# Performance work log

Measured on AMD Instinct MI355X. Metric: run time of the kernel, lower is better.

The kernel has to match this reference:

```python
import jax, jax.numpy as jnp
import numpy as np

D = 1024
EXPAND = 2
DI = EXPAND * D
K = 4           # d_conv
C = 64          # chunk_size
ALPHA = 0.9     # memory decay
B, S = 2, 8192
EPS = 1e-5


def setup_inputs() -> dict:
    key = jax.random.key(0)
    ks = jax.random.split(key, 10)
    s = 0.02
    return {
        "x": jax.random.normal(ks[0], (B, S, D), dtype=jnp.float32),
        "norm_w": jnp.ones((D,), dtype=jnp.float32),
        "w_up": jax.random.normal(ks[1], (D, DI), dtype=jnp.float32) * s,
        "w_gate": jax.random.normal(ks[2], (D, DI), dtype=jnp.float32) * s,
        "w_down": jax.random.normal(ks[3], (DI, D), dtype=jnp.float32) * s,
        "conv_w": jax.random.normal(ks[4], (K, 1, DI), dtype=jnp.float32) * s,  # WIO depthwise
        "conv_b": jnp.zeros((DI,), dtype=jnp.float32),
        "wq": jax.random.normal(ks[5], (D, D), dtype=jnp.float32) * s,
        "wk": jax.random.normal(ks[6], (D, D), dtype=jnp.float32) * s,
        "wv": jax.random.normal(ks[7], (D, D), dtype=jnp.float32) * s,
        "wo": jax.random.normal(ks[8], (D, D), dtype=jnp.float32) * s,
    }


def _rmsnorm(x, w):
    ms = jnp.mean(jnp.square(x.astype(jnp.float32)), axis=-1, keepdims=True)
    return (x * jax.lax.rsqrt(ms + EPS).astype(x.dtype)) * w


def _causal_depthwise_conv(u, conv_w, conv_b):
    # u: [B,S,DI]; depthwise causal conv over S, then SiLU
    y = jax.lax.conv_general_dilated(
        u, conv_w,
        window_strides=(1,), padding=[(K - 1, 0)],
        dimension_numbers=("NWC", "WIO", "NWC"),
        feature_group_count=DI)
    return jax.nn.silu(y + conv_b)


def _hebbian_memory(h, wq, wk, wv, wo):
    # chunked linear-attention style Hebbian memory
    b, s, d = h.shape
    n = s // C
    scale = d ** -0.5
    q = (h @ wq).reshape(b, n, C, d) * scale
    k = (h @ wk).reshape(b, n, C, d)
    v = (h @ wv).reshape(b, n, C, d)
    mask = jnp.tril(jnp.ones((C, C), dtype=h.dtype))  # inclusive causal within chunk

    def step(M, qkv):
        qc, kc, vc = qkv  # [b,C,d]
        inter = jnp.einsum("bcd,bde->bce", qc, M)
        attn = jnp.einsum("bcd,bed->bce", qc, kc) * mask
        intra = jnp.einsum("bce,bed->bcd", attn, vc)
        M_new = ALPHA * M + jnp.einsum("bcd,bce->bde", kc, vc)
        return M_new, inter + intra

    M0 = jnp.zeros((b, d, d), dtype=h.dtype)
    qkv = (jnp.swapaxes(q, 0, 1), jnp.swapaxes(k, 0, 1), jnp.swapaxes(v, 0, 1))
    _, o = jax.lax.scan(step, M0, qkv)        # [n,b,C,d]
    o = jnp.swapaxes(o, 0, 1).reshape(b, s, d)
    return o @ wo


def reference(x, norm_w, w_up, w_gate, w_down, conv_w, conv_b, wq, wk, wv, wo):
    normed = _rmsnorm(x, norm_w)
    val = _causal_depthwise_conv(normed @ w_up, conv_w, conv_b)   # [B,S,DI]
    gate = jax.nn.silu(normed @ w_gate)
    out = (gate * val) @ w_down                                   # [B,S,D]
    out = _hebbian_memory(out, wq, wk, wv, wo)
    return x + out
```

## Files before the change

### kernel.cpp

```cpp
#include <hip/hip_runtime.h>
#include <cstdint>
#include <cstddef>

#define SS 8192
#define DD 1024
#define DI2 2048
#define NR 16384

#define LOG2_09 (-0.152003093445050f)
#define LAMBDA16 0.185302018885184f

typedef __attribute__((ext_vector_type(4))) float f32x4;
typedef __attribute__((ext_vector_type(8))) __bf16 bf16x8;

union U16 { uint4 u; bf16x8 b; };

static __device__ __forceinline__ f32x4 MFMA(uint4 a, uint4 b, f32x4 c) {
  U16 ua, ub; ua.u = a; ub.u = b;
  return __builtin_amdgcn_mfma_f32_16x16x32_bf16(ua.b, ub.b, c, 0, 0, 0);
}

static __device__ __forceinline__ unsigned short f2bf(float f) {
  union { float f; unsigned u; } v; v.f = f;
  return (unsigned short)((v.u + 0x7FFFu + ((v.u >> 16) & 1u)) >> 16);
}
static __device__ __forceinline__ float bf2f(unsigned b) {
  union { unsigned u; float f; } v; v.u = b << 16; return v.f;
}
static __device__ __forceinline__ void unpack8(uint4 u, float* f) {
  f[0] = bf2f(u.x & 0xFFFFu); f[1] = bf2f(u.x >> 16);
  f[2] = bf2f(u.y & 0xFFFFu); f[3] = bf2f(u.y >> 16);
  f[4] = bf2f(u.z & 0xFFFFu); f[5] = bf2f(u.z >> 16);
  f[6] = bf2f(u.w & 0xFFFFu); f[7] = bf2f(u.w >> 16);
}

static __device__ __forceinline__ void glds16(const unsigned short* g, char* l) {
  __builtin_amdgcn_global_load_lds(
      (const __attribute__((address_space(1))) unsigned int*)g,
      (__attribute__((address_space(3))) unsigned int*)l, 16, 0, 0);
}

__global__ __launch_bounds__(256)
void transpose_cast(const float* __restrict__ in, unsigned short* __restrict__ out, int R, int Cc) {
  __shared__ float tile[32][33];
  const int r0 = blockIdx.y * 32, c0 = blockIdx.x * 32;
  const int tx = threadIdx.x, ty = threadIdx.y;
#pragma unroll
  for (int i = 0; i < 4; i++)
    tile[ty + i * 8][tx] = in[(size_t)(r0 + ty + i * 8) * Cc + c0 + tx];
  __syncthreads();
#pragma unroll
  for (int i = 0; i < 4; i++)
    out[(size_t)(c0 + ty + i * 8) * R + r0 + tx] = f2bf(tile[tx][ty + i * 8]);
}

__global__ __launch_bounds__(256)
void rmsnorm_kernel(const float* __restrict__ x, const float* __restrict__ w,
                    unsigned short* __restrict__ out) {
  const int row = blockIdx.x, t = threadIdx.x;
  const float4 v = ((const float4*)(x + (size_t)row * DD))[t];
  float ss = v.x * v.x + v.y * v.y + v.z * v.z + v.w * v.w;
  __shared__ float sred[256];
  sred[t] = ss;
  __syncthreads();
  for (int o = 128; o > 0; o >>= 1) {
    if (t < o) sred[t] += sred[t + o];
    __syncthreads();
  }
  const float rr = rsqrtf(sred[0] * (1.0f / (float)DD) + 1e-5f);
  const float4 wv = ((const float4*)w)[t];
  uint2 pk;
  pk.x = (unsigned)f2bf(v.x * rr * wv.x) | ((unsigned)f2bf(v.y * rr * wv.y) << 16);
  pk.y = (unsigned)f2bf(v.z * rr * wv.z) | ((unsigned)f2bf(v.w * rr * wv.w) << 16);
  *(uint2*)(out + (size_t)row * DD + t * 4) = pk;
}

enum { EP_BF16 = 0, EP_BF16_BOTH = 1, EP_BF16_T = 2, EP_F32_RES = 3, EP_STATE = 4,
       EP_CROSS = 5, EP_SCORE = 6, EP_PV = 7, EP_QKV = 8 };

template <int MODE>
__global__ __launch_bounds__(512, 2)
void gemm256(const unsigned short* __restrict__ A, const unsigned short* __restrict__ Bt,
             unsigned short* __restrict__ Cb, unsigned short* __restrict__ Ct,
             float* __restrict__ Cf, const float* __restrict__ resid,
             int M, int N, int kLen, int lda, int ldb, float scale) {
  __shared__ char sLds[131072];
  const int t = threadIdx.x, lane = t & 63, wid = t >> 6;
  const int wr = wid >> 2, wc = wid & 3;
  const int l15 = lane & 15, lh = lane >> 4;
  const int mblocks = M >> 8;
  int m0, n0;
  if constexpr (MODE == EP_SCORE) {
    const int p = (int)blockIdx.x;
    const int mt = (p >= 6) ? 3 : (p >= 3) ? 2 : (p >= 1) ? 1 : 0;
    const int nt = p - ((mt * (mt + 1)) >> 1);
    m0 = mt << 8; n0 = nt << 8;
  } else if ((mblocks & 7) == 0) {
    const int msl = mblocks >> 3;
    const int xcd = (int)blockIdx.x & 7, loc = (int)blockIdx.x >> 3;
    m0 = (xcd * msl + (loc % msl)) << 8;
    n0 = (loc / msl) << 8;
  } else {
    m0 = ((int)blockIdx.x % mblocks) << 8;
    n0 = ((int)blockIdx.x / mblocks) << 8;
  }
  int zb = 0, zg = 0;
  const unsigned short* Abase = A;
  const unsigned short* Bbase = Bt;
  if constexpr (MODE == EP_STATE || MODE == EP_CROSS || MODE == EP_SCORE || MODE == EP_PV) {
    const int gb = blockIdx.z;
    zb = gb >> 3; zg = gb & 7;
    if constexpr (MODE == EP_STATE) {
      Abase = A + (size_t)zb * DD * SS + (size_t)zg * 1024;
      Bbase = Bt + (size_t)zb * DD * SS + (size_t)zg * 1024;
    } else if constexpr (MODE == EP_CROSS) {
      Abase = A + ((size_t)zb * SS + (size_t)zg * 1024) * (size_t)lda;
      Bbase = Bt + ((size_t)blockIdx.z << 20);
    } else if constexpr (MODE == EP_SCORE) {
      Abase = A + ((size_t)zb * SS + (size_t)zg * 1024) * (size_t)lda;
      Bbase = Bt + ((size_t)zb * SS + (size_t)zg * 1024) * (size_t)ldb;
    } else {
      Abase = A + ((size_t)blockIdx.z << 20);
      Bbase = Bt + (size_t)zb * DD * SS + (size_t)zg * 1024;
    }
  }
  const int srow = wid * 16 + (lane >> 2);
  const int scol = ((lane & 3) << 3) ^ (((srow >> 1) & 3) << 3);
  const unsigned short* pA0 = Abase + (size_t)(m0 + srow) * lda + scol;
  const unsigned short* pA1 = pA0 + (size_t)128 * lda;
  const unsigned short* pB0 = Bbase + (size_t)(n0 + srow) * ldb + scol;
  const unsigned short* pB1 = pB0 + (size_t)128 * ldb;
  const int ldsW = wid * 1024;
  int offA[8], offB[4];
#pragma unroll
  for (int mf = 0; mf < 8; mf++) {
    const int r = wr * 128 + mf * 16 + l15;
    offA[mf] = r * 64 + ((lh * 16) ^ (((r >> 1) & 3) << 4));
  }
#pragma unroll
  for (int nf = 0; nf < 4; nf++) {
    const int r = wc * 64 + nf * 16 + l15;
    offB[nf] = r * 64 + ((lh * 16) ^ (((r >> 1) & 3) << 4));
  }
  int NT = kLen >> 5;
  if constexpr (MODE == EP_PV) NT = ((m0 >> 8) + 1) << 3;
#define BUFA(tt) (sLds + ((tt) & 3) * 32768)
#define BUFB(tt) (sLds + ((tt) & 3) * 32768 + 16384)
#define STAGEA(tt) do { const int _k = (tt) * 32; \
    glds16(pA0 + _k, BUFA(tt) + ldsW); \
    glds16(pA1 + _k, BUFA(tt) + 8192 + ldsW); } while (0)
#define STAGEB(tt) do { const int _k = (tt) * 32; \
    glds16(pB0 + _k, BUFB(tt) + ldsW); \
    glds16(pB1 + _k, BUFB(tt) + 8192 + ldsW); } while (0)
  STAGEA(0); STAGEB(0); STAGEA(1); STAGEB(1); STAGEA(2); STAGEB(2);
  asm volatile("s_waitcnt vmcnt(8)" ::: "memory");
  __builtin_amdgcn_s_barrier();
  f32x4 acc[8][4] = {};
  for (int kt = 0; kt < NT; ++kt) {
    const char* At  = BUFA(kt);
    const char* Bt_ = BUFB(kt);
    uint4 av[8], bv[4];
#pragma unroll
    for (int i = 0; i < 8; i++) av[i] = *(const uint4*)(At + offA[i]);
#pragma unroll
    for (int i = 0; i < 4; i++) bv[i] = *(const uint4*)(Bt_ + offB[i]);
    if (kt + 3 < NT) { STAGEA(kt + 3); STAGEB(kt + 3); }
    __builtin_amdgcn_s_setprio(1);
#pragma unroll
    for (int mf = 0; mf < 8; mf++)
#pragma unroll
      for (int nf = 0; nf < 4; nf++)
        acc[mf][nf] = MFMA(av[mf], bv[nf], acc[mf][nf]);
    __builtin_amdgcn_s_setprio(0);
    if (kt < NT - 3)       { asm volatile("s_waitcnt vmcnt(8)" ::: "memory"); }
    else if (kt == NT - 3) { asm volatile("s_waitcnt vmcnt(4)" ::: "memory"); }
    else if (kt == NT - 2) { asm volatile("s_waitcnt vmcnt(0)" ::: "memory"); }
    __builtin_amdgcn_s_barrier();
  }
#undef STAGEA
#undef STAGEB
#undef BUFA
#undef BUFB
#pragma unroll
  for (int mf = 0; mf < 8; mf++) {
    const int r0 = m0 + wr * 128 + mf * 16 + lh * 4;
#pragma unroll
    for (int nf = 0; nf < 4; nf++) {
      const int c = n0 + wc * 64 + nf * 16 + l15;
      f32x4 v = acc[mf][nf] * scale;
      if constexpr (MODE == EP_F32_RES) {
#pragma unroll
        for (int jj = 0; jj < 4; jj++) {
          const size_t idx = (size_t)(r0 + jj) * N + c;
          Cf[idx] = v[jj] + resid[idx];
        }
      } else if constexpr (MODE == EP_STATE) {
        unsigned short* Tg = Cb + ((size_t)blockIdx.z << 20);
#pragma unroll
        for (int jj = 0; jj < 4; jj++)
          Tg[(size_t)(r0 + jj) * 1024 + c] = f2bf(v[jj]);
      } else if constexpr (MODE == EP_CROSS) {
        const float rs = exp2f((float)(r0 >> 6) * LOG2_09);
#pragma unroll
        for (int jj = 0; jj < 4; jj++) {
          const size_t idx = ((size_t)zb * SS + (size_t)zg * 1024 + r0 + jj) * DD + c;
          Cb[idx] = f2bf(bf2f(Cb[idx]) + v[jj] * rs);
        }
      } else if constexpr (MODE == EP_SCORE) {
        unsigned short* Sg = Cb + ((size_t)blockIdx.z << 20);
        const int qt = r0 >> 6;
        const int tb = c >> 6;
        float w;
        if (tb > qt)       w = 0.0f;
        else if (tb == qt) w = 1.0f;
        else               w = exp2f((float)(qt - 1 - tb) * LOG2_09);
#pragma unroll
        for (int jj = 0; jj < 4; jj++) {
          float val = v[jj] * w;
          if (tb == qt && (c & 63) > ((r0 + jj) & 63)) val = 0.0f;
          Sg[(size_t)(r0 + jj) * 1024 + c] = f2bf(val);
        }
      } else if constexpr (MODE == EP_PV) {
#pragma unroll
        for (int jj = 0; jj < 4; jj++)
          Cb[((size_t)zb * SS + (size_t)zg * 1024 + r0 + jj) * DD + c] = f2bf(v[jj]);
      } else if constexpr (MODE == EP_QKV) {
        unsigned short* qb  = Cb;
        unsigned short* kb  = Ct;
        unsigned short* ktb = (unsigned short*)Cf;
        unsigned short* vtb = (unsigned short*)const_cast<float*>(resid);
        const int sect = c >> 10, cc = c & 1023;
        const int bb = r0 >> 13, s0 = r0 & (SS - 1);
        if (sect == 0) {
#pragma unroll
          for (int jj = 0; jj < 4; jj++)
            qb[(size_t)(r0 + jj) * DD + cc] = f2bf(v[jj] * 0.03125f);
        } else if (sect == 1) {
#pragma unroll
          for (int jj = 0; jj < 4; jj++)
            kb[(size_t)(r0 + jj) * DD + cc] = f2bf(v[jj]);
          const float wt = exp2f((float)(15 - ((s0 >> 6) & 15)) * LOG2_09);
          uint2 pk;
          pk.x = (unsigned)f2bf(v[0] * wt) | ((unsigned)f2bf(v[1] * wt) << 16);
          pk.y = (unsigned)f2bf(v[2] * wt) | ((unsigned)f2bf(v[3] * wt) << 16);
          *(uint2*)(ktb + ((size_t)bb * DD + cc) * SS + s0) = pk;
        } else {
          uint2 pk;
          pk.x = (unsigned)f2bf(v[0]) | ((unsigned)f2bf(v[1]) << 16);
          pk.y = (unsigned)f2bf(v[2]) | ((unsigned)f2bf(v[3]) << 16);
          *(uint2*)(vtb + ((size_t)bb * DD + cc) * SS + s0) = pk;
        }
      } else {
        if constexpr (MODE == EP_BF16 || MODE == EP_BF16_BOTH) {
#pragma unroll
          for (int jj = 0; jj < 4; jj++)
            Cb[(size_t)(r0 + jj) * N + c] = f2bf(v[jj]);
        }
        if constexpr (MODE == EP_BF16_BOTH || MODE == EP_BF16_T) {
          const int bb = r0 >> 13, s0 = r0 & (SS - 1);
          float wt = 1.0f;
          if constexpr (MODE == EP_BF16_BOTH)
            wt = exp2f((float)(15 - ((s0 >> 6) & 15)) * LOG2_09);
          uint2 pk;
          pk.x = (unsigned)f2bf(v[0] * wt) | ((unsigned)f2bf(v[1] * wt) << 16);
          pk.y = (unsigned)f2bf(v[2] * wt) | ((unsigned)f2bf(v[3] * wt) << 16);
          *(uint2*)(Ct + ((size_t)bb * DD + c) * SS + s0) = pk;
        }
      }
    }
  }
}

__global__ __launch_bounds__(256)
void convgate_kernel(const unsigned short* __restrict__ ug, const float* __restrict__ cw,
                     const float* __restrict__ cb, unsigned short* __restrict__ hin) {
  const int r = blockIdx.x;
  const int c0 = threadIdx.x * 8;
  const int s = r & (SS - 1);
  float acc[8];
#pragma unroll
  for (int i = 0; i < 8; i++) acc[i] = cb[c0 + i];
  for (int tap = 0; tap < 4; tap++) {
    const int ds = s - 3 + tap;
    if (ds < 0) continue;
    uint4 uv = *(const uint4*)(ug + (size_t)(r - 3 + tap) * 4096 + c0);
    float u[8]; unpack8(uv, u);
#pragma unroll
    for (int i = 0; i < 8; i++) acc[i] += u[i] * cw[tap * DI2 + c0 + i];
  }
  uint4 gv = *(const uint4*)(ug + (size_t)r * 4096 + DI2 + c0);
  float gt[8]; unpack8(gv, gt);
  unsigned short o16[8];
#pragma unroll
  for (int i = 0; i < 8; i++) {
    const float val = acc[i] / (1.0f + __expf(-acc[i]));
    const float gg  = gt[i] / (1.0f + __expf(-gt[i]));
    o16[i] = f2bf(val * gg);
  }
  uint4 ov;
  ov.x = (unsigned)o16[0] | ((unsigned)o16[1] << 16);
  ov.y = (unsigned)o16[2] | ((unsigned)o16[3] << 16);
  ov.z = (unsigned)o16[4] | ((unsigned)o16[5] << 16);
  ov.w = (unsigned)o16[6] | ((unsigned)o16[7] << 16);
  *(uint4*)(hin + (size_t)r * DI2 + c0) = ov;
}

__global__ __launch_bounds__(256)
void prefix_kernel(unsigned short* __restrict__ Tb) {
  const int tid = blockIdx.x * 256 + threadIdx.x;
  const int b = tid >> 17, i = tid & 131071;
  unsigned short* p = Tb + (((size_t)b * 8) << 20) + (size_t)i * 8;
  float acc[8] = {};
  for (int g = 0; g < 8; g++) {
    unsigned short* pg = p + ((size_t)g << 20);
    uint4 tv = *(uint4*)pg;
    float tf_[8]; unpack8(tv, tf_);
    uint4 ov;
    ov.x = (unsigned)f2bf(acc[0]) | ((unsigned)f2bf(acc[1]) << 16);
    ov.y = (unsigned)f2bf(acc[2]) | ((unsigned)f2bf(acc[3]) << 16);
    ov.z = (unsigned)f2bf(acc[4]) | ((unsigned)f2bf(acc[5]) << 16);
    ov.w = (unsigned)f2bf(acc[6]) | ((unsigned)f2bf(acc[7]) << 16);
    *(uint4*)pg = ov;
#pragma unroll
    for (int e = 0; e < 8; e++) acc[e] = LAMBDA16 * acc[e] + tf_[e];
  }
}

extern "C" void kernel_launch(void* const* d_in, const int* in_sizes, int n_in,
                              void* d_out, int out_size, void* d_ws, size_t ws_size,
                              hipStream_t stream) {
  (void)in_sizes; (void)n_in; (void)out_size;
  const float* x      = (const float*)d_in[0];
  const float* norm_w = (const float*)d_in[1];
  const float* w_up   = (const float*)d_in[2];
  const float* w_gate = (const float*)d_in[3];
  const float* w_down = (const float*)d_in[4];
  const float* conv_w = (const float*)d_in[5];
  const float* conv_b = (const float*)d_in[6];
  const float* wq     = (const float*)d_in[7];
  const float* wk     = (const float*)d_in[8];
  const float* wv     = (const float*)d_in[9];
  const float* wo     = (const float*)d_in[10];
  float* out = (float*)d_out;

  const size_t MB = 1ull << 20;
  if (ws_size < 212 * MB) return;
  char* base = (char*)d_ws;
  unsigned short* ug     = (unsigned short*)(base + 0);
  unsigned short* hbuf   = (unsigned short*)(base + 0);
  unsigned short* Tbuf   = (unsigned short*)(base + 0);
  unsigned short* qbuf   = (unsigned short*)(base + 32 * MB);
  unsigned short* kbuf   = (unsigned short*)(base + 64 * MB);
  unsigned short* ktbuf  = (unsigned short*)(base + 96 * MB);
  unsigned short* sbuf   = (unsigned short*)(base + 96 * MB);
  unsigned short* normed = (unsigned short*)(base + 128 * MB);
  unsigned short* hin    = (unsigned short*)(base + 128 * MB);
  unsigned short* vtbuf  = (unsigned short*)(base + 128 * MB);
  unsigned short* obuf   = (unsigned short*)(base + 160 * MB);
  unsigned short* wugt   = (unsigned short*)(base + 192 * MB);
  unsigned short* wdt    = (unsigned short*)(base + 200 * MB);
  unsigned short* wqkvt  = (unsigned short*)(base + 204 * MB);
  unsigned short* wot    = (unsigned short*)(base + 210 * MB);

  dim3 tb(32, 8);
  transpose_cast<<<dim3(DI2 / 32, DD / 32), tb, 0, stream>>>(w_up,   wugt,                    DD,  DI2);
  transpose_cast<<<dim3(DI2 / 32, DD / 32), tb, 0, stream>>>(w_gate, wugt + (size_t)DI2 * DD, DD,  DI2);
  transpose_cast<<<dim3(DD / 32, DI2 / 32), tb, 0, stream>>>(w_down, wdt, DI2, DD);
  transpose_cast<<<dim3(DD / 32, DD / 32),  tb, 0, stream>>>(wq, wqkvt,                          DD, DD);
  transpose_cast<<<dim3(DD / 32, DD / 32),  tb, 0, stream>>>(wk, wqkvt + (size_t)DD * DD,       DD, DD);
  transpose_cast<<<dim3(DD / 32, DD / 32),  tb, 0, stream>>>(wv, wqkvt + (size_t)2 * DD * DD,   DD, DD);
  transpose_cast<<<dim3(DD / 32, DD / 32),  tb, 0, stream>>>(wo, wot, DD, DD);

  rmsnorm_kernel<<<NR, 256, 0, stream>>>(x, norm_w, normed);

  gemm256<EP_BF16><<<dim3((NR / 256) * (4096 / 256)), 512, 0, stream>>>(
      normed, wugt, ug, nullptr, nullptr, nullptr, NR, 4096, DD, DD, DD, 1.0f);

  convgate_kernel<<<NR, 256, 0, stream>>>(ug, conv_w, conv_b, hin);

  gemm256<EP_BF16><<<dim3((NR / 256) * (DD / 256)), 512, 0, stream>>>(
      hin, wdt, hbuf, nullptr, nullptr, nullptr, NR, DD, DI2, DI2, DI2, 1.0f);

  gemm256<EP_QKV><<<dim3((NR / 256) * (3072 / 256)), 512, 0, stream>>>(
      hbuf, wqkvt, qbuf, kbuf, (float*)ktbuf, (const float*)vtbuf,
      NR, 3072, DD, DD, DD, 1.0f);

  gemm256<EP_STATE><<<dim3(16, 1, 16), 512, 0, stream>>>(
      vtbuf, ktbuf, Tbuf, nullptr, nullptr, nullptr, 1024, 1024, 1024, SS, SS, 1.0f);
  gemm256<EP_SCORE><<<dim3(10, 1, 16), 512, 0, stream>>>(
      qbuf, kbuf, sbuf, nullptr, nullptr, nullptr, 1024, 1024, 1024, DD, DD, 1.0f);
  prefix_kernel<<<1024, 256, 0, stream>>>(Tbuf);
  gemm256<EP_PV><<<dim3(16, 1, 16), 512, 0, stream>>>(
      sbuf, vtbuf, obuf, nullptr, nullptr, nullptr, 1024, 1024, 1024, 1024, SS, 1.0f);
  gemm256<EP_CROSS><<<dim3(16, 1, 16), 512, 0, stream>>>(
      qbuf, Tbuf, obuf, nullptr, nullptr, nullptr, 1024, 1024, 1024, DD, 1024, 1.0f);

  gemm256<EP_F32_RES><<<dim3((NR / 256) * (DD / 256)), 512, 0, stream>>>(
      obuf, wot, nullptr, nullptr, out, x, NR, DD, DD, DD, DD, 1.0f);
}
```

Baseline: 669.1 us.

## Fuse cross-group state GEMM into PV GEMM by concatenating K dimension

The separate EP_CROSS GEMM, which read-modify-wrote the output with a decay-scaled q·T product, is folded into the PV GEMM. The K loop is extended by 32 tiles that stage a pre-decayed q copy and the prefix state instead of scores and V. To make this work, the QKV epilogue now also writes a decay-weighted scaled q (qsbuf). This removes one kernel launch and the bf16 read-modify-write pass over the output, at the cost of an extra q write and some buffer reassignments that reuse workspace regions.

```diff
diff --git a/kernel.cpp b/kernel.cpp
--- a/kernel.cpp
+++ b/kernel.cpp
@@ -76,13 +76,14 @@
 }
 
 enum { EP_BF16 = 0, EP_BF16_BOTH = 1, EP_BF16_T = 2, EP_F32_RES = 3, EP_STATE = 4,
-       EP_CROSS = 5, EP_SCORE = 6, EP_PV = 7, EP_QKV = 8 };
+       EP_SCORE = 6, EP_PVX = 7, EP_QKV = 8 };
 
 template <int MODE>
 __global__ __launch_bounds__(512, 2)
 void gemm256(const unsigned short* __restrict__ A, const unsigned short* __restrict__ Bt,
              unsigned short* __restrict__ Cb, unsigned short* __restrict__ Ct,
              float* __restrict__ Cf, const float* __restrict__ resid,
+             unsigned short* __restrict__ Cx,
              int M, int N, int kLen, int lda, int ldb, float scale) {
   __shared__ char sLds[131072];
   const int t = threadIdx.x, lane = t & 63, wid = t >> 6;
@@ -107,15 +108,12 @@
   int zb = 0, zg = 0;
   const unsigned short* Abase = A;
   const unsigned short* Bbase = Bt;
-  if constexpr (MODE == EP_STATE || MODE == EP_CROSS || MODE == EP_SCORE || MODE == EP_PV) {
+  if constexpr (MODE == EP_STATE || MODE == EP_SCORE || MODE == EP_PVX) {
     const int gb = blockIdx.z;
     zb = gb >> 3; zg = gb & 7;
     if constexpr (MODE == EP_STATE) {
       Abase = A + (size_t)zb * DD * SS + (size_t)zg * 1024;
       Bbase = Bt + (size_t)zb * DD * SS + (size_t)zg * 1024;
-    } else if constexpr (MODE == EP_CROSS) {
-      Abase = A + ((size_t)zb * SS + (size_t)zg * 1024) * (size_t)lda;
-      Bbase = Bt + ((size_t)blockIdx.z << 20);
     } else if constexpr (MODE == EP_SCORE) {
       Abase = A + ((size_t)zb * SS + (size_t)zg * 1024) * (size_t)lda;
       Bbase = Bt + ((size_t)zb * SS + (size_t)zg * 1024) * (size_t)ldb;
@@ -131,6 +129,17 @@
   const unsigned short* pB0 = Bbase + (size_t)(n0 + srow) * ldb + scol;
   const unsigned short* pB1 = pB0 + (size_t)128 * ldb;
   const int ldsW = wid * 1024;
+  int ntV = 0;
+  const unsigned short *pA2 = nullptr, *pA2h = nullptr, *pB2 = nullptr, *pB2h = nullptr;
+  if constexpr (MODE == EP_PVX) {
+    ntV = ((m0 >> 8) + 1) << 3;
+    const unsigned short* qsb = Cx + ((size_t)zb * SS + (size_t)zg * 1024) * DD;
+    pA2  = qsb + (size_t)(m0 + srow) * DD + scol;
+    pA2h = pA2 + (size_t)128 * DD;
+    const unsigned short* mnb = Ct + ((size_t)blockIdx.z << 20);
+    pB2  = mnb + (size_t)(n0 + srow) * 1024 + scol;
+    pB2h = pB2 + (size_t)128 * 1024;
+  }
   int offA[8], offB[4];
 #pragma unroll
   for (int mf = 0; mf < 8; mf++) {
@@ -143,16 +152,28 @@
     offB[nf] = r * 64 + ((lh * 16) ^ (((r >> 1) & 3) << 4));
   }
   int NT = kLen >> 5;
-  if constexpr (MODE == EP_PV) NT = ((m0 >> 8) + 1) << 3;
+  if constexpr (MODE == EP_PVX) NT = ntV + 32;
 #define BUFA(tt) (sLds + ((tt) & 3) * 32768)
 #define BUFB(tt) (sLds + ((tt) & 3) * 32768 + 16384)
-#define STAGEA(tt) do { const int _k = (tt) * 32; \
-    glds16(pA0 + _k, BUFA(tt) + ldsW); \
-    glds16(pA1 + _k, BUFA(tt) + 8192 + ldsW); } while (0)
-#define STAGEB(tt) do { const int _k = (tt) * 32; \
-    glds16(pB0 + _k, BUFB(tt) + ldsW); \
-    glds16(pB1 + _k, BUFB(tt) + 8192 + ldsW); } while (0)
-  STAGEA(0); STAGEB(0); STAGEA(1); STAGEB(1); STAGEA(2); STAGEB(2);
+  auto stage = [&](int tt) {
+    const int _k = tt * 32;
+    const unsigned short* a0 = pA0 + _k;
+    const unsigned short* a1 = pA1 + _k;
+    const unsigned short* b0 = pB0 + _k;
+    const unsigned short* b1 = pB1 + _k;
+    if constexpr (MODE == EP_PVX) {
+      if (tt >= ntV) {
+        const int k2 = (tt - ntV) * 32;
+        a0 = pA2 + k2; a1 = pA2h + k2;
+        b0 = pB2 + k2; b1 = pB2h + k2;
+      }
+    }
+    glds16(a0, BUFA(tt) + ldsW);
+    glds16(a1, BUFA(tt) + 8192 + ldsW);
+    glds16(b0, BUFB(tt) + ldsW);
+    glds16(b1, BUFB(tt) + 8192 + ldsW);
+  };
+  stage(0); stage(1); stage(2);
   asm volatile("s_waitcnt vmcnt(8)" ::: "memory");
   __builtin_amdgcn_s_barrier();
   f32x4 acc[8][4] = {};
@@ -164,7 +185,7 @@
     for (int i = 0; i < 8; i++) av[i] = *(const uint4*)(At + offA[i]);
 #pragma unroll
     for (int i = 0; i < 4; i++) bv[i] = *(const uint4*)(Bt_ + offB[i]);
-    if (kt + 3 < NT) { STAGEA(kt + 3); STAGEB(kt + 3); }
+    if (kt + 3 < NT) stage(kt + 3);
     __builtin_amdgcn_s_setprio(1);
 #pragma unroll
     for (int mf = 0; mf < 8; mf++)
@@ -177,8 +198,6 @@
     else if (kt == NT - 2) { asm volatile("s_waitcnt vmcnt(0)" ::: "memory"); }
     __builtin_amdgcn_s_barrier();
   }
-#undef STAGEA
-#undef STAGEB
 #undef BUFA
 #undef BUFB
 #pragma unroll
@@ -199,13 +218,6 @@
 #pragma unroll
         for (int jj = 0; jj < 4; jj++)
           Tg[(size_t)(r0 + jj) * 1024 + c] = f2bf(v[jj]);
-      } else if constexpr (MODE == EP_CROSS) {
-        const float rs = exp2f((float)(r0 >> 6) * LOG2_09);
-#pragma unroll
-        for (int jj = 0; jj < 4; jj++) {
-          const size_t idx = ((size_t)zb * SS + (size_t)zg * 1024 + r0 + jj) * DD + c;
-          Cb[idx] = f2bf(bf2f(Cb[idx]) + v[jj] * rs);
-        }
       } else if constexpr (MODE == EP_SCORE) {
         unsigned short* Sg = Cb + ((size_t)blockIdx.z << 20);
         const int qt = r0 >> 6;
@@ -220,7 +232,7 @@
           if (tb == qt && (c & 63) > ((r0 + jj) & 63)) val = 0.0f;
           Sg[(size_t)(r0 + jj) * 1024 + c] = f2bf(val);
         }
-      } else if constexpr (MODE == EP_PV) {
+      } else if constexpr (MODE == EP_PVX) {
 #pragma unroll
         for (int jj = 0; jj < 4; jj++)
           Cb[((size_t)zb * SS + (size_t)zg * 1024 + r0 + jj) * DD + c] = f2bf(v[jj]);
@@ -232,9 +244,12 @@
         const int sect = c >> 10, cc = c & 1023;
         const int bb = r0 >> 13, s0 = r0 & (SS - 1);
         if (sect == 0) {
-#pragma unroll
-          for (int jj = 0; jj < 4; jj++)
+          const float wq_row = exp2f((float)((s0 >> 6) & 15) * LOG2_09);
+#pragma unroll
+          for (int jj = 0; jj < 4; jj++) {
             qb[(size_t)(r0 + jj) * DD + cc] = f2bf(v[jj] * 0.03125f);
+            Cx[(size_t)(r0 + jj) * DD + cc] = f2bf(v[jj] * 0.03125f * wq_row);
+          }
         } else if (sect == 1) {
 #pragma unroll
           for (int jj = 0; jj < 4; jj++)
@@ -351,12 +366,13 @@
   unsigned short* Tbuf   = (unsigned short*)(base + 0);
   unsigned short* qbuf   = (unsigned short*)(base + 32 * MB);
   unsigned short* kbuf   = (unsigned short*)(base + 64 * MB);
+  unsigned short* obuf   = (unsigned short*)(base + 64 * MB);
   unsigned short* ktbuf  = (unsigned short*)(base + 96 * MB);
   unsigned short* sbuf   = (unsigned short*)(base + 96 * MB);
   unsigned short* normed = (unsigned short*)(base + 128 * MB);
   unsigned short* hin    = (unsigned short*)(base + 128 * MB);
   unsigned short* vtbuf  = (unsigned short*)(base + 128 * MB);
-  unsigned short* obuf   = (unsigned short*)(base + 160 * MB);
+  unsigned short* qsbuf  = (unsigned short*)(base + 160 * MB);
   unsigned short* wugt   = (unsigned short*)(base + 192 * MB);
   unsigned short* wdt    = (unsigned short*)(base + 200 * MB);
   unsigned short* wqkvt  = (unsigned short*)(base + 204 * MB);
@@ -374,27 +390,28 @@
   rmsnorm_kernel<<<NR, 256, 0, stream>>>(x, norm_w, normed);
 
   gemm256<EP_BF16><<<dim3((NR / 256) * (4096 / 256)), 512, 0, stream>>>(
-      normed, wugt, ug, nullptr, nullptr, nullptr, NR, 4096, DD, DD, DD, 1.0f);
+      normed, wugt, ug, nullptr, nullptr, nullptr, nullptr, NR, 4096, DD, DD, DD, 1.0f);
 
   convgate_kernel<<<NR, 256, 0, stream>>>(ug, conv_w, conv_b, hin);
 
   gemm256<EP_BF16><<<dim3((NR / 256) * (DD / 256)), 512, 0, stream>>>(
-      hin, wdt, hbuf, nullptr, nullptr, nullptr, NR, DD, DI2, DI2, DI2, 1.0f);
+      hin, wdt, hbuf, nullptr, nullptr, nullptr, nullptr, NR, DD, DI2, DI2, DI2, 1.0f);
 
   gemm256<EP_QKV><<<dim3((NR / 256) * (3072 / 256)), 512, 0, stream>>>(
-      hbuf, wqkvt, qbuf, kbuf, (float*)ktbuf, (const float*)vtbuf,
+      hbuf, wqkvt, qbuf, kbuf, (float*)ktbuf, (const float*)vtbuf, qsbuf,
       NR, 3072, DD, DD, DD, 1.0f);
 
   gemm256<EP_STATE><<<dim3(16, 1, 16), 512, 0, stream>>>(
-      vtbuf, ktbuf, Tbuf, nullptr, nullptr, nullptr, 1024, 1024, 1024, SS, SS, 1.0f);
+      vtbuf, ktbuf, Tbuf, nullptr, nullptr, nullptr, nullptr,
+      1024, 1024, 1024, SS, SS, 1.0f);
   gemm256<EP_SCORE><<<dim3(10, 1, 16), 512, 0, stream>>>(
-      qbuf, kbuf, sbuf, nullptr, nullptr, nullptr, 1024, 1024, 1024, DD, DD, 1.0f);
+      qbuf, kbuf, sbuf, nullptr, nullptr, nullptr, nullptr,
+      1024, 1024, 1024, DD, DD, 1.0f);
   prefix_kernel<<<1024, 256, 0, stream>>>(Tbuf);
-  gemm256<EP_PV><<<dim3(16, 1, 16), 512, 0, stream>>>(
-      sbuf, vtbuf, obuf, nullptr, nullptr, nullptr, 1024, 1024, 1024, 1024, SS, 1.0f);
-  gemm256<EP_CROSS><<<dim3(16, 1, 16), 512, 0, stream>>>(
-      qbuf, Tbuf, obuf, nullptr, nullptr, nullptr, 1024, 1024, 1024, DD, 1024, 1.0f);
+  gemm256<EP_PVX><<<dim3(16, 1, 16), 512, 0, stream>>>(
+      sbuf, vtbuf, obuf, Tbuf, nullptr, nullptr, qsbuf,
+      1024, 1024, 1024, 1024, SS, 1.0f);
 
   gemm256<EP_F32_RES><<<dim3((NR / 256) * (DD / 256)), 512, 0, stream>>>(
-      obuf, wot, nullptr, nullptr, out, x, NR, DD, DD, DD, DD, 1.0f);
-}
+      obuf, wot, nullptr, nullptr, out, x, nullptr, NR, DD, DD, DD, DD, 1.0f);
+}
```

Result: faster. 644.3 us (median of 2 runs) (-3.7%).
